# Optimization experiments

Measured on AMD Instinct MI355X. Metric: run time of the kernel, lower is better.

Reference implementation:

```python
import jax, jax.numpy as jnp
import numpy as np
import math

EMBED_DIM = 768
NUM_HEADS = 12
HEAD_DIM = EMBED_DIM // NUM_HEADS
EPS = 1e-6


def setup_inputs() -> dict:
    key = jax.random.key(0)
    ks = jax.random.split(key, 9)
    T, B, N, D = 4, 4, 1024, EMBED_DIM
    s = 0.02
    return {
        "x": jax.random.normal(ks[0], (T, B, N, D), dtype=jnp.float32),
        "Wq": jax.random.normal(ks[1], (D, D), dtype=jnp.float32) * s,
        "bq": jax.random.normal(ks[2], (D,), dtype=jnp.float32) * s,
        "Wk": jax.random.normal(ks[3], (D, D), dtype=jnp.float32) * s,
        "bk": jax.random.normal(ks[4], (D,), dtype=jnp.float32) * s,
        "Wv": jax.random.normal(ks[5], (D, D), dtype=jnp.float32) * s,
        "bv": jax.random.normal(ks[6], (D,), dtype=jnp.float32) * s,
        "Wo": jax.random.normal(ks[7], (D, D), dtype=jnp.float32) * s,
        "bo": jax.random.normal(ks[8], (D,), dtype=jnp.float32) * s,
    }


def _split_heads(y, T, B, N):
    # [T,B,N,D] -> [T,B,H,N,Dh]
    return y.reshape(T, B, N, NUM_HEADS, HEAD_DIM).transpose(0, 1, 3, 2, 4)


def reference(x, Wq, bq, Wk, bk, Wv, bv, Wo, bo):
    T, B, N, D = x.shape
    # q/k/v projections (nn.Linear: x @ W^T + b)
    q = _split_heads(x @ Wq.T + bq, T, B, N)
    k = _split_heads(x @ Wk.T + bk, T, B, N)
    v = _split_heads(x @ Wv.T + bv, T, B, N)
    # scores = q k^T / sqrt(head_dim)
    scores = jnp.einsum("tbhnd,tbhmd->tbhnm", q, k) / math.sqrt(HEAD_DIM)
    # spike-form normalization: relu then L1-normalize along keys
    act = jax.nn.relu(scores)
    attn = act / (act.sum(axis=-1, keepdims=True) + EPS)
    ctx = jnp.einsum("tbhnm,tbhmd->tbhnd", attn, v)
    # merge heads: [T,B,H,N,Dh] -> [T,B,N,D]
    out = ctx.transpose(0, 1, 3, 2, 4).reshape(T, B, N, D)
    return out @ Wo.T + bo
```

## Files before the change

kernel.cpp:

```cpp
#include <hip/hip_runtime.h>
#include <hip/hip_bf16.h>
#include <cstdint>


typedef __attribute__((ext_vector_type(8))) short short8;
typedef __attribute__((ext_vector_type(4))) float float4v;
typedef __attribute__((ext_vector_type(16))) float float16v;

__device__ __forceinline__ unsigned short f2bf(float f) {
  unsigned int u = __float_as_uint(f);
  u = (u + 0x7fffu + ((u >> 16) & 1u)) >> 16;
  return (unsigned short)u;
}

__device__ __forceinline__ unsigned int pkbf(float a, float b) {
  unsigned int ua = __float_as_uint(a) + 0x8000u;
  unsigned int ub = __float_as_uint(b) + 0x8000u;
  return __builtin_amdgcn_perm(ub, ua, 0x07060302u);
}

__device__ __forceinline__ void gld_lds16(const void* g, void* lds) {
  __builtin_amdgcn_global_load_lds(
      (__attribute__((address_space(1))) void*)(uintptr_t)g,
      (__attribute__((address_space(3))) void*)(uint32_t)(uintptr_t)lds,
      16, 0, 0);
}

__global__ __launch_bounds__(256) void cast_all(
    const float* __restrict__ x,  const float* __restrict__ Wq,
    const float* __restrict__ Wk, const float* __restrict__ Wv,
    const float* __restrict__ Wo, unsigned short* __restrict__ XBF,
    unsigned short* __restrict__ WQKV, unsigned short* __restrict__ WOb) {
  const int bid = blockIdx.x;
  const float* src;
  unsigned short* dst;
  int i;
  if (bid < 12288) {
    src = x; dst = XBF; i = bid * 256 + threadIdx.x;
  } else {
    const int wb = bid - 12288;
    const int which = wb / 576;
    i = (wb % 576) * 256 + threadIdx.x;
    src = (which == 0) ? Wq : (which == 1) ? Wk : (which == 2) ? Wv : Wo;
    dst = (which == 0) ? WQKV
        : (which == 1) ? WQKV + 589824
        : (which == 2) ? WQKV + 1179648 : WOb;
  }
  float4 f = reinterpret_cast<const float4*>(src)[i];
  ushort4 o;
  o.x = f2bf(f.x); o.y = f2bf(f.y); o.z = f2bf(f.z); o.w = f2bf(f.w);
  reinterpret_cast<ushort4*>(dst)[i] = o;
}

__global__ __launch_bounds__(512) void gemm256(
    const unsigned short* __restrict__ A,
    const unsigned short* __restrict__ Bt,
    unsigned short* __restrict__ Cb,
    unsigned short* __restrict__ Vt,
    const float* __restrict__ b0, const float* __restrict__ b1,
    const float* __restrict__ b2) {
  constexpr int K = 768;
  constexpr int KT = 24;
  __shared__ unsigned short Ab[2][256 * 32];
  __shared__ unsigned short Bb[2][256 * 32];

  const int tid = threadIdx.x;
  const int lane = tid & 63;
  const int wv = tid >> 6;
  const int wm = wv >> 2, wn = wv & 3;
  const int l15 = lane & 15, quad = lane >> 4;

  const int gx = gridDim.x;
  const int nwg = gx * gridDim.y;
  const int hw = blockIdx.y * gx + blockIdx.x;
  const int per = nwg >> 3;
  const int lg = (hw & 7) * per + (hw >> 3);
  const int bx = lg % gx, by = lg / gx;
  const int i0 = by * 256, j0 = bx * 256;

  const int srow = tid >> 2;
  const int scol = ((tid & 3) << 3) ^ ((srow & 6) << 2);
  const unsigned short* pa0 = A  + (size_t)(i0 + srow) * K + scol;
  const unsigned short* pb0 = Bt + (size_t)(j0 + srow) * K + scol;
  const int xsw = ((quad * 8) ^ ((l15 & 6) * 4));
  const int aoff = (wm * 128 + l15) * 32 + xsw;
  const int boff = (wn * 64 + l15) * 32 + xsw;

  auto stA = [&](int kt, int bb, int h) {
    gld_lds16(pa0 + (size_t)h * 128 * K + kt * 32,
              &Ab[bb][h * 4096 + wv * 512]);
  };
  auto stB = [&](int kt, int bb, int h) {
    gld_lds16(pb0 + (size_t)h * 128 * K + kt * 32,
              &Bb[bb][h * 4096 + wv * 512]);
  };

  float4v acc[8][4];
#pragma unroll
  for (int m = 0; m < 8; ++m)
#pragma unroll
    for (int n = 0; n < 4; ++n) acc[m][n] = float4v{0.f, 0.f, 0.f, 0.f};

  stB(0, 0, 0); stB(0, 0, 1);
  stA(0, 0, 0); stA(0, 0, 1);
  stB(1, 1, 0); stB(1, 1, 1);
  asm volatile("s_waitcnt vmcnt(2)" ::: "memory");
  __builtin_amdgcn_s_barrier();
  __builtin_amdgcn_sched_barrier(0);

#pragma unroll 1
  for (int t = 0; t < KT; ++t) {
    const int bb = t & 1, nb = bb ^ 1;
    short8 bf[4];
    short8 a0, a1;

#pragma unroll
    for (int fn = 0; fn < 4; ++fn)
      bf[fn] = *(const short8*)&Bb[bb][boff + fn * 512];
    a0 = *(const short8*)&Ab[bb][aoff + 0 * 512];
    a1 = *(const short8*)&Ab[bb][aoff + 1 * 512];
    if (t + 1 < KT) stA(t + 1, nb, 0);
    __builtin_amdgcn_s_barrier();
    asm volatile("s_waitcnt lgkmcnt(0)" ::: "memory");
    __builtin_amdgcn_sched_barrier(0);
    __builtin_amdgcn_s_setprio(1);
#pragma unroll
    for (int fn = 0; fn < 4; ++fn)
      acc[0][fn] = __builtin_amdgcn_mfma_f32_16x16x32_bf16(a0, bf[fn], acc[0][fn], 0, 0, 0);
#pragma unroll
    for (int fn = 0; fn < 4; ++fn)
      acc[1][fn] = __builtin_amdgcn_mfma_f32_16x16x32_bf16(a1, bf[fn], acc[1][fn], 0, 0, 0);
    __builtin_amdgcn_s_setprio(0);
    __builtin_amdgcn_s_barrier();

    a0 = *(const short8*)&Ab[bb][aoff + 2 * 512];
    a1 = *(const short8*)&Ab[bb][aoff + 3 * 512];
    if (t + 1 < KT) stA(t + 1, nb, 1);
    __builtin_amdgcn_s_barrier();
    asm volatile("s_waitcnt lgkmcnt(0)" ::: "memory");
    __builtin_amdgcn_sched_barrier(0);
    __builtin_amdgcn_s_setprio(1);
#pragma unroll
    for (int fn = 0; fn < 4; ++fn)
      acc[2][fn] = __builtin_amdgcn_mfma_f32_16x16x32_bf16(a0, bf[fn], acc[2][fn], 0, 0, 0);
#pragma unroll
    for (int fn = 0; fn < 4; ++fn)
      acc[3][fn] = __builtin_amdgcn_mfma_f32_16x16x32_bf16(a1, bf[fn], acc[3][fn], 0, 0, 0);
    __builtin_amdgcn_s_setprio(0);
    __builtin_amdgcn_s_barrier();

    a0 = *(const short8*)&Ab[bb][aoff + 4 * 512];
    a1 = *(const short8*)&Ab[bb][aoff + 5 * 512];
    if (t + 2 < KT) stB(t + 2, bb, 0);
    __builtin_amdgcn_s_barrier();
    asm volatile("s_waitcnt lgkmcnt(0)" ::: "memory");
    __builtin_amdgcn_sched_barrier(0);
    __builtin_amdgcn_s_setprio(1);
#pragma unroll
    for (int fn = 0; fn < 4; ++fn)
      acc[4][fn] = __builtin_amdgcn_mfma_f32_16x16x32_bf16(a0, bf[fn], acc[4][fn], 0, 0, 0);
#pragma unroll
    for (int fn = 0; fn < 4; ++fn)
      acc[5][fn] = __builtin_amdgcn_mfma_f32_16x16x32_bf16(a1, bf[fn], acc[5][fn], 0, 0, 0);
    __builtin_amdgcn_s_setprio(0);
    __builtin_amdgcn_s_barrier();

    a0 = *(const short8*)&Ab[bb][aoff + 6 * 512];
    a1 = *(const short8*)&Ab[bb][aoff + 7 * 512];
    if (t + 2 < KT) stB(t + 2, bb, 1);
    __builtin_amdgcn_s_barrier();
    asm volatile("s_waitcnt lgkmcnt(0)" ::: "memory");
    __builtin_amdgcn_sched_barrier(0);
    __builtin_amdgcn_s_setprio(1);
#pragma unroll
    for (int fn = 0; fn < 4; ++fn)
      acc[6][fn] = __builtin_amdgcn_mfma_f32_16x16x32_bf16(a0, bf[fn], acc[6][fn], 0, 0, 0);
#pragma unroll
    for (int fn = 0; fn < 4; ++fn)
      acc[7][fn] = __builtin_amdgcn_mfma_f32_16x16x32_bf16(a1, bf[fn], acc[7][fn], 0, 0, 0);
    __builtin_amdgcn_s_setprio(0);
    if (t + 2 < KT) {
      asm volatile("s_waitcnt vmcnt(2)" ::: "memory");
      __builtin_amdgcn_s_barrier();
      __builtin_amdgcn_sched_barrier(0);
    } else if (t + 1 < KT) {
      asm volatile("s_waitcnt vmcnt(0)" ::: "memory");
      __builtin_amdgcn_s_barrier();
      __builtin_amdgcn_sched_barrier(0);
    }
  }

  const int sel = bx / 3;
  const float* bp = (sel == 0) ? b0 : ((sel == 1) ? b1 : b2);
#pragma unroll
  for (int fm = 0; fm < 8; ++fm) {
    const int row0 = i0 + wm * 128 + fm * 16 + quad * 4;
#pragma unroll
    for (int fn = 0; fn < 4; ++fn) {
      const int col = j0 + wn * 64 + fn * 16 + l15;
      const float bias = bp[col - sel * 768];
      if (sel == 2) {
        const int tb = row0 >> 10;
        const int n0 = row0 & 1023;
        const int hd = col - 1536;
        const float v0 = acc[fm][fn][0] + bias;
        const float v1 = acc[fm][fn][1] + bias;
        const float v2 = acc[fm][fn][2] + bias;
        const float v3 = acc[fm][fn][3] + bias;
        uint2 u;
        u.x = (unsigned int)f2bf(v0) | ((unsigned int)f2bf(v1) << 16);
        u.y = (unsigned int)f2bf(v2) | ((unsigned int)f2bf(v3) << 16);
        *(uint2*)&Vt[((size_t)(tb * 768 + hd)) * 1024 + n0] = u;
      } else {
#pragma unroll
        for (int r = 0; r < 4; ++r)
          Cb[(size_t)(row0 + r) * 2304 + col] = f2bf(acc[fm][fn][r] + bias);
      }
    }
  }
}

__global__ __launch_bounds__(256) void gemm_bt(
    const unsigned short* __restrict__ A,
    const unsigned short* __restrict__ Bt,
    float* __restrict__ Cf,
    const float* __restrict__ b0, int N) {
  constexpr int K = 768;
  constexpr int KT = K / 32;
  __shared__ unsigned short As[3][128 * 32];
  __shared__ unsigned short Bs[3][128 * 32];

  const int tid = threadIdx.x;
  const int lane = tid & 63;
  const int w = tid >> 6;
  const int wrow = w >> 1, wcol = w & 1;
  const int l15 = lane & 15, quad = lane >> 4;

  const int gx = gridDim.x;
  const int nwg = gx * gridDim.y;
  const int hw = blockIdx.y * gx + blockIdx.x;
  const int per = nwg >> 3;
  const int lg = (hw & 7) * per + (hw >> 3);
  const int bx = lg % gx, by = lg / gx;
  const int i0 = by * 128, j0 = bx * 128;

  const unsigned short* ga = A + (size_t)(i0 + 32 * w + (lane >> 2)) * K + (lane & 3) * 8;
  const unsigned short* gb = Bt + (size_t)(j0 + 32 * w + (lane >> 2)) * K + (lane & 3) * 8;

  auto stage = [&](int kt2, int bufi) {
    const unsigned short* pa = ga + kt2 * 32;
    const unsigned short* pb = gb + kt2 * 32;
    gld_lds16(pa, &As[bufi][(32 * w) * 32]);
    gld_lds16(pa + 16 * K, &As[bufi][(32 * w + 16) * 32]);
    gld_lds16(pb, &Bs[bufi][(32 * w) * 32]);
    gld_lds16(pb + 16 * K, &Bs[bufi][(32 * w + 16) * 32]);
  };

  float4v acc[4][4];
#pragma unroll
  for (int a = 0; a < 4; ++a)
#pragma unroll
    for (int b = 0; b < 4; ++b) acc[a][b] = float4v{0.f, 0.f, 0.f, 0.f};

  stage(0, 0);
  stage(1, 1);
  asm volatile("s_waitcnt vmcnt(4)" ::: "memory");
  __builtin_amdgcn_s_barrier();
  __builtin_amdgcn_sched_barrier(0);

#pragma unroll 1
  for (int kt = 0; kt < KT; ++kt) {
    const int cur = kt % 3;
    if (kt + 2 < KT) stage(kt + 2, (kt + 2) % 3);

    short8 af[4], bfr[4];
#pragma unroll
    for (int a = 0; a < 4; ++a)
      af[a] = *(const short8*)&As[cur][(wrow * 64 + a * 16 + l15) * 32 + quad * 8];
#pragma unroll
    for (int b = 0; b < 4; ++b)
      bfr[b] = *(const short8*)&Bs[cur][(wcol * 64 + b * 16 + l15) * 32 + quad * 8];
#pragma unroll
    for (int a = 0; a < 4; ++a)
#pragma unroll
      for (int b = 0; b < 4; ++b)
        acc[a][b] = __builtin_amdgcn_mfma_f32_16x16x32_bf16(af[a], bfr[b], acc[a][b], 0, 0, 0);

    if (kt + 2 < KT) {
      asm volatile("s_waitcnt vmcnt(4)" ::: "memory");
      __builtin_amdgcn_s_barrier();
      __builtin_amdgcn_sched_barrier(0);
    } else if (kt + 1 < KT) {
      asm volatile("s_waitcnt vmcnt(0)" ::: "memory");
      __builtin_amdgcn_s_barrier();
      __builtin_amdgcn_sched_barrier(0);
    }
  }

#pragma unroll
  for (int a = 0; a < 4; ++a) {
    const int row0 = i0 + wrow * 64 + a * 16 + quad * 4;
#pragma unroll
    for (int b = 0; b < 4; ++b) {
      const int col = j0 + wcol * 64 + b * 16 + l15;
      const float bias = b0[col];
#pragma unroll
      for (int r = 0; r < 4; ++r)
        Cf[(size_t)(row0 + r) * N + col] = acc[a][b][r] + bias;
    }
  }
}

__global__ __launch_bounds__(256) void attn32(
    const unsigned short* __restrict__ qkv,
    const unsigned short* __restrict__ vt,
    unsigned short* __restrict__ ctx) {
  __shared__ unsigned short Ks[2][64 * 72];
  __shared__ unsigned short Vs[2][64 * 72];

  const int tbh = blockIdx.x;
  const int qt = blockIdx.y;
  const int tb = tbh / 12, h = tbh % 12;
  const int tid = threadIdx.x, lane = tid & 63, w = tid >> 6;
  const int l31 = lane & 31, hl = lane >> 5;

  short8 qf[2][4];
#pragma unroll
  for (int qs = 0; qs < 2; ++qs) {
    const unsigned short* qp =
        qkv + (size_t)(tb * 1024 + qt * 256 + w * 64 + qs * 32 + l31) * 2304 +
        h * 64 + hl * 8;
#pragma unroll
    for (int kc = 0; kc < 4; ++kc) qf[qs][kc] = *(const short8*)(qp + kc * 16);
  }

  const int srow = tid >> 3;
  const int sblk = tid & 7;
  const unsigned short* kcol =
      qkv + (size_t)(tb * 1024) * 2304 + 768 + h * 64 + sblk * 8;
  const unsigned short* vcol = vt + ((size_t)tbh * 64 + srow) * 1024 + sblk * 8;
  uint4 kr0, kr1, vr0, vr1;
  auto loadKV = [&](int kv) {
    const unsigned short* kp = kcol + (size_t)(kv * 64 + srow) * 2304;
    kr0 = *(const uint4*)kp;
    kr1 = *(const uint4*)(kp + 32 * 2304);
    const unsigned short* vp = vcol + kv * 64;
    vr0 = *(const uint4*)vp;
    vr1 = *(const uint4*)(vp + 32 * 1024);
  };

  float16v octx[2][2];
#pragma unroll
  for (int qs = 0; qs < 2; ++qs)
#pragma unroll
    for (int dt = 0; dt < 2; ++dt)
#pragma unroll
      for (int i = 0; i < 16; ++i) octx[qs][dt][i] = 0.f;
  float den[2] = {0.f, 0.f};

  loadKV(0);

#pragma unroll 1
  for (int kv = 0; kv < 16; ++kv) {
    const int cur = kv & 1;
    *(uint4*)&Ks[cur][srow * 72 + sblk * 8] = kr0;
    *(uint4*)&Ks[cur][(srow + 32) * 72 + sblk * 8] = kr1;
    *(uint4*)&Vs[cur][srow * 72 + sblk * 8] = vr0;
    *(uint4*)&Vs[cur][(srow + 32) * 72 + sblk * 8] = vr1;
    if (kv < 15) loadKV(kv + 1);
    asm volatile("s_waitcnt lgkmcnt(0)" ::: "memory");
    __builtin_amdgcn_s_barrier();
    __builtin_amdgcn_sched_barrier(0);

#pragma unroll
    for (int qs = 0; qs < 2; ++qs) {
      unsigned int pk[2][8];
#pragma unroll
      for (int mt = 0; mt < 2; ++mt) {
        float16v st;
#pragma unroll
        for (int i = 0; i < 16; ++i) st[i] = 0.f;
#pragma unroll
        for (int kc = 0; kc < 4; ++kc) {
          short8 kf =
              *(const short8*)&Ks[cur][(mt * 32 + l31) * 72 + kc * 16 + hl * 8];
          st = __builtin_amdgcn_mfma_f32_32x32x16_bf16(kf, qf[qs][kc], st, 0, 0, 0);
        }
#pragma unroll
        for (int g = 0; g < 4; ++g) {
          float v0 = st[4 * g + 0]; v0 = v0 > 0.f ? v0 : 0.f;
          float v1 = st[4 * g + 1]; v1 = v1 > 0.f ? v1 : 0.f;
          float v2 = st[4 * g + 2]; v2 = v2 > 0.f ? v2 : 0.f;
          float v3 = st[4 * g + 3]; v3 = v3 > 0.f ? v3 : 0.f;
          den[qs] += (v0 + v1) + (v2 + v3);
          pk[mt][g * 2 + 0] = pkbf(v0, v1);
          pk[mt][g * 2 + 1] = pkbf(v2, v3);
        }
      }
#pragma unroll
      for (int kc = 0; kc < 4; ++kc) {
        const int mt = kc >> 1, gb = (kc & 1) * 2;
        unsigned int a0 = pk[mt][gb * 2 + 0], b0 = pk[mt][gb * 2 + 2];
        unsigned int a1 = pk[mt][gb * 2 + 1], b1 = pk[mt][gb * 2 + 3];
        asm("v_permlane32_swap_b32 %0, %1" : "+v"(a0), "+v"(b0));
        asm("v_permlane32_swap_b32 %0, %1" : "+v"(a1), "+v"(b1));
        union { unsigned int u[4]; short8 s; } pf;
        pf.u[0] = a0; pf.u[1] = a1; pf.u[2] = b0; pf.u[3] = b1;
#pragma unroll
        for (int dt = 0; dt < 2; ++dt) {
          short8 vb =
              *(const short8*)&Vs[cur][(dt * 32 + l31) * 72 + kc * 16 + hl * 8];
          octx[qs][dt] = __builtin_amdgcn_mfma_f32_32x32x16_bf16(
              vb, pf.s, octx[qs][dt], 0, 0, 0);
        }
      }
    }
  }

#pragma unroll
  for (int qs = 0; qs < 2; ++qs) {
    float d = den[qs] + __shfl_xor(den[qs], 32);
    const float sc = 1.f / (d + 8e-6f);
    const size_t qrow = (size_t)(tb * 1024 + qt * 256 + w * 64 + qs * 32 + l31);
#pragma unroll
    for (int dt = 0; dt < 2; ++dt)
#pragma unroll
      for (int g = 0; g < 4; ++g) {
        const float v0 = octx[qs][dt][4 * g + 0] * sc;
        const float v1 = octx[qs][dt][4 * g + 1] * sc;
        const float v2 = octx[qs][dt][4 * g + 2] * sc;
        const float v3 = octx[qs][dt][4 * g + 3] * sc;
        uint2 u;
        u.x = pkbf(v0, v1);
        u.y = pkbf(v2, v3);
        *(uint2*)&ctx[qrow * 768 + h * 64 + dt * 32 + g * 8 + hl * 4] = u;
      }
  }
}

extern "C" void kernel_launch(void* const* d_in, const int* in_sizes, int n_in,
                              void* d_out, int out_size, void* d_ws, size_t ws_size,
                              hipStream_t stream) {
  const float* x  = (const float*)d_in[0];
  const float* Wq = (const float*)d_in[1];
  const float* bq = (const float*)d_in[2];
  const float* Wk = (const float*)d_in[3];
  const float* bk = (const float*)d_in[4];
  const float* Wv = (const float*)d_in[5];
  const float* bv = (const float*)d_in[6];
  const float* Wo = (const float*)d_in[7];
  const float* bo = (const float*)d_in[8];
  float* out = (float*)d_out;

  char* ws = (char*)d_ws;
  unsigned short* XBF  = (unsigned short*)(ws);
  unsigned short* CTX  = (unsigned short*)(ws);
  unsigned short* WQKV = (unsigned short*)(ws + 25165824);
  unsigned short* WOb  = (unsigned short*)(ws + 28704768);
  unsigned short* QKV  = (unsigned short*)(ws + 29884416);
  unsigned short* VT   = (unsigned short*)(ws + 105381888);

  cast_all<<<14592, 256, 0, stream>>>(x, Wq, Wk, Wv, Wo, XBF, WQKV, WOb);

  gemm256<<<dim3(9, 64), 512, 0, stream>>>(XBF, WQKV, QKV, VT, bq, bk, bv);
  attn32<<<dim3(192, 4), 256, 0, stream>>>(QKV, VT, CTX);
  gemm_bt<<<dim3(6, 128), 256, 0, stream>>>(CTX, WOb, out, bo, 768);
}
```

Baseline: 315.6 us.

## Double GEMM K-tile depth to 64 with wider XOR swizzle

The 256x256 projection GEMM now stages 64-wide K slices per iteration instead of 32, halving the main-loop trip count and the number of barriers per unit of work. The LDS layout changes to 64-element rows with an 8-way XOR swizzle, and each phase issues two global-to-LDS loads and twice as many MFMAs. This doubles LDS use to 128 KB per block, which may limit occupancy and raises register pressure from holding more B fragments.

```diff
diff --git a/kernel.cpp b/kernel.cpp
--- a/kernel.cpp
+++ b/kernel.cpp
@@ -60,15 +60,16 @@
     const float* __restrict__ b0, const float* __restrict__ b1,
     const float* __restrict__ b2) {
   constexpr int K = 768;
-  constexpr int KT = 24;
-  __shared__ unsigned short Ab[2][256 * 32];
-  __shared__ unsigned short Bb[2][256 * 32];
+  constexpr int KT = 12;
+  __shared__ unsigned short Ab[2][256 * 64];
+  __shared__ unsigned short Bb[2][256 * 64];
 
   const int tid = threadIdx.x;
   const int lane = tid & 63;
   const int wv = tid >> 6;
   const int wm = wv >> 2, wn = wv & 3;
   const int l15 = lane & 15, quad = lane >> 4;
+  const int xr = l15 & 7;
 
   const int gx = gridDim.x;
   const int nwg = gx * gridDim.y;
@@ -78,21 +79,18 @@
   const int bx = lg % gx, by = lg / gx;
   const int i0 = by * 256, j0 = bx * 256;
 
-  const int srow = tid >> 2;
-  const int scol = ((tid & 3) << 3) ^ ((srow & 6) << 2);
+  const int srow = tid >> 3;
+  const int scol = ((tid & 7) * 8) ^ ((srow & 7) * 8);
   const unsigned short* pa0 = A  + (size_t)(i0 + srow) * K + scol;
   const unsigned short* pb0 = Bt + (size_t)(j0 + srow) * K + scol;
-  const int xsw = ((quad * 8) ^ ((l15 & 6) * 4));
-  const int aoff = (wm * 128 + l15) * 32 + xsw;
-  const int boff = (wn * 64 + l15) * 32 + xsw;
-
-  auto stA = [&](int kt, int bb, int h) {
-    gld_lds16(pa0 + (size_t)h * 128 * K + kt * 32,
-              &Ab[bb][h * 4096 + wv * 512]);
+
+  auto stA = [&](int kt, int bb_, int h) {
+    gld_lds16(pa0 + (size_t)h * 64 * K + kt * 64,
+              &Ab[bb_][h * 4096 + wv * 512]);
   };
-  auto stB = [&](int kt, int bb, int h) {
-    gld_lds16(pb0 + (size_t)h * 128 * K + kt * 32,
-              &Bb[bb][h * 4096 + wv * 512]);
+  auto stB = [&](int kt, int bb_, int h) {
+    gld_lds16(pb0 + (size_t)h * 64 * K + kt * 64,
+              &Bb[bb_][h * 4096 + wv * 512]);
   };
 
   float4v acc[8][4];
@@ -101,92 +99,70 @@
 #pragma unroll
     for (int n = 0; n < 4; ++n) acc[m][n] = float4v{0.f, 0.f, 0.f, 0.f};
 
-  stB(0, 0, 0); stB(0, 0, 1);
-  stA(0, 0, 0); stA(0, 0, 1);
-  stB(1, 1, 0); stB(1, 1, 1);
-  asm volatile("s_waitcnt vmcnt(2)" ::: "memory");
+  stB(0, 0, 0); stB(0, 0, 1); stB(0, 0, 2); stB(0, 0, 3);
+  stA(0, 0, 0); stA(0, 0, 1); stA(0, 0, 2); stA(0, 0, 3);
+  stB(1, 1, 0); stB(1, 1, 1); stB(1, 1, 2); stB(1, 1, 3);
+  asm volatile("s_waitcnt vmcnt(4)" ::: "memory");
   __builtin_amdgcn_s_barrier();
   __builtin_amdgcn_sched_barrier(0);
 
 #pragma unroll 1
   for (int t = 0; t < KT; ++t) {
-    const int bb = t & 1, nb = bb ^ 1;
-    short8 bf[4];
-    short8 a0, a1;
-
-#pragma unroll
-    for (int fn = 0; fn < 4; ++fn)
-      bf[fn] = *(const short8*)&Bb[bb][boff + fn * 512];
-    a0 = *(const short8*)&Ab[bb][aoff + 0 * 512];
-    a1 = *(const short8*)&Ab[bb][aoff + 1 * 512];
-    if (t + 1 < KT) stA(t + 1, nb, 0);
-    __builtin_amdgcn_s_barrier();
-    asm volatile("s_waitcnt lgkmcnt(0)" ::: "memory");
-    __builtin_amdgcn_sched_barrier(0);
-    __builtin_amdgcn_s_setprio(1);
-#pragma unroll
-    for (int fn = 0; fn < 4; ++fn)
-      acc[0][fn] = __builtin_amdgcn_mfma_f32_16x16x32_bf16(a0, bf[fn], acc[0][fn], 0, 0, 0);
-#pragma unroll
-    for (int fn = 0; fn < 4; ++fn)
-      acc[1][fn] = __builtin_amdgcn_mfma_f32_16x16x32_bf16(a1, bf[fn], acc[1][fn], 0, 0, 0);
-    __builtin_amdgcn_s_setprio(0);
-    __builtin_amdgcn_s_barrier();
-
-    a0 = *(const short8*)&Ab[bb][aoff + 2 * 512];
-    a1 = *(const short8*)&Ab[bb][aoff + 3 * 512];
-    if (t + 1 < KT) stA(t + 1, nb, 1);
-    __builtin_amdgcn_s_barrier();
-    asm volatile("s_waitcnt lgkmcnt(0)" ::: "memory");
-    __builtin_amdgcn_sched_barrier(0);
-    __builtin_amdgcn_s_setprio(1);
-#pragma unroll
-    for (int fn = 0; fn < 4; ++fn)
-      acc[2][fn] = __builtin_amdgcn_mfma_f32_16x16x32_bf16(a0, bf[fn], acc[2][fn], 0, 0, 0);
-#pragma unroll
-    for (int fn = 0; fn < 4; ++fn)
-      acc[3][fn] = __builtin_amdgcn_mfma_f32_16x16x32_bf16(a1, bf[fn], acc[3][fn], 0, 0, 0);
-    __builtin_amdgcn_s_setprio(0);
-    __builtin_amdgcn_s_barrier();
-
-    a0 = *(const short8*)&Ab[bb][aoff + 4 * 512];
-    a1 = *(const short8*)&Ab[bb][aoff + 5 * 512];
-    if (t + 2 < KT) stB(t + 2, bb, 0);
-    __builtin_amdgcn_s_barrier();
-    asm volatile("s_waitcnt lgkmcnt(0)" ::: "memory");
-    __builtin_amdgcn_sched_barrier(0);
-    __builtin_amdgcn_s_setprio(1);
-#pragma unroll
-    for (int fn = 0; fn < 4; ++fn)
-      acc[4][fn] = __builtin_amdgcn_mfma_f32_16x16x32_bf16(a0, bf[fn], acc[4][fn], 0, 0, 0);
-#pragma unroll
-    for (int fn = 0; fn < 4; ++fn)
-      acc[5][fn] = __builtin_amdgcn_mfma_f32_16x16x32_bf16(a1, bf[fn], acc[5][fn], 0, 0, 0);
-    __builtin_amdgcn_s_setprio(0);
-    __builtin_amdgcn_s_barrier();
-
-    a0 = *(const short8*)&Ab[bb][aoff + 6 * 512];
-    a1 = *(const short8*)&Ab[bb][aoff + 7 * 512];
-    if (t + 2 < KT) stB(t + 2, bb, 1);
-    __builtin_amdgcn_s_barrier();
-    asm volatile("s_waitcnt lgkmcnt(0)" ::: "memory");
-    __builtin_amdgcn_sched_barrier(0);
-    __builtin_amdgcn_s_setprio(1);
-#pragma unroll
-    for (int fn = 0; fn < 4; ++fn)
-      acc[6][fn] = __builtin_amdgcn_mfma_f32_16x16x32_bf16(a0, bf[fn], acc[6][fn], 0, 0, 0);
-#pragma unroll
-    for (int fn = 0; fn < 4; ++fn)
-      acc[7][fn] = __builtin_amdgcn_mfma_f32_16x16x32_bf16(a1, bf[fn], acc[7][fn], 0, 0, 0);
-    __builtin_amdgcn_s_setprio(0);
-    if (t + 2 < KT) {
-      asm volatile("s_waitcnt vmcnt(2)" ::: "memory");
+    const int bb_ = t & 1, nb = bb_ ^ 1;
+    short8 bfq[4][2];
+
+#pragma unroll
+    for (int p = 0; p < 4; ++p) {
+      short8 a0[2], a1[2];
+#pragma unroll
+      for (int ks = 0; ks < 2; ++ks) {
+        if (p == 0) {
+#pragma unroll
+          for (int fn = 0; fn < 4; ++fn)
+            bfq[fn][ks] = *(const short8*)
+                &Bb[bb_][(wn * 64 + fn * 16 + l15) * 64 +
+                         (((ks * 4 + quad) ^ xr) * 8)];
+        }
+        a0[ks] = *(const short8*)
+            &Ab[bb_][(wm * 128 + (2 * p) * 16 + l15) * 64 +
+                     (((ks * 4 + quad) ^ xr) * 8)];
+        a1[ks] = *(const short8*)
+            &Ab[bb_][(wm * 128 + (2 * p + 1) * 16 + l15) * 64 +
+                     (((ks * 4 + quad) ^ xr) * 8)];
+      }
+      if (p < 2) {
+        if (t + 1 < KT) { stA(t + 1, nb, 2 * p); stA(t + 1, nb, 2 * p + 1); }
+      } else {
+        if (t + 2 < KT) { stB(t + 2, bb_, 2 * (p - 2)); stB(t + 2, bb_, 2 * (p - 2) + 1); }
+      }
       __builtin_amdgcn_s_barrier();
+      asm volatile("s_waitcnt lgkmcnt(0)" ::: "memory");
       __builtin_amdgcn_sched_barrier(0);
-    } else if (t + 1 < KT) {
-      asm volatile("s_waitcnt vmcnt(0)" ::: "memory");
-      __builtin_amdgcn_s_barrier();
-      __builtin_amdgcn_sched_barrier(0);
+      __builtin_amdgcn_s_setprio(1);
+#pragma unroll
+      for (int ks = 0; ks < 2; ++ks) {
+#pragma unroll
+        for (int fn = 0; fn < 4; ++fn) {
+          acc[2 * p][fn] = __builtin_amdgcn_mfma_f32_16x16x32_bf16(
+              a0[ks], bfq[fn][ks], acc[2 * p][fn], 0, 0, 0);
+          acc[2 * p + 1][fn] = __builtin_amdgcn_mfma_f32_16x16x32_bf16(
+              a1[ks], bfq[fn][ks], acc[2 * p + 1][fn], 0, 0, 0);
+        }
+      }
+      __builtin_amdgcn_s_setprio(0);
+      if (p < 3) {
+        __builtin_amdgcn_s_barrier();
+      } else {
+        if (t + 2 < KT) {
+          asm volatile("s_waitcnt vmcnt(4)" ::: "memory");
+          __builtin_amdgcn_s_barrier();
+          __builtin_amdgcn_sched_barrier(0);
+        } else if (t + 1 < KT) {
+          asm volatile("s_waitcnt vmcnt(0)" ::: "memory");
+          __builtin_amdgcn_s_barrier();
+          __builtin_amdgcn_sched_barrier(0);
+        }
+      }
     }
   }
 
```

Result: faster. 308.4 us (-2.3%).
